# Kernel tuning notes

Hardware: AMD Instinct MI355X
Metric: run time of the kernel (lower is better)

Reference implementation:

```python
import jax, jax.numpy as jnp
import numpy as np

LOG2 = float(np.log(2.0))
N_NODES = 100000

def ssp(x):
    return jax.nn.softplus(x) - LOG2

def _xavier(key, out_dim, in_dim):
    bound = float(np.sqrt(6.0 / (in_dim + out_dim)))
    return jax.random.uniform(key, (out_dim, in_dim), jnp.float32, -bound, bound)

def setup_inputs() -> dict:
    key = jax.random.key(0)
    ks = jax.random.split(key, 10)
    H, F = 128, 128  # hidden_channels, num_filters
    C2 = int(2 * H * 0.5)          # lin2 out = 128
    C2h = int(2 * H) - C2          # lin2_hull out = 128
    E, Eh = 1600000, 400000
    v = jax.random.normal(ks[0], (N_NODES, H), jnp.float32)
    e = jax.random.normal(ks[1], (E, F), jnp.float32)
    edge_index = jax.random.randint(ks[2], (2, E), 0, N_NODES, jnp.int64)
    e_hull = jax.random.normal(ks[3], (Eh, F), jnp.float32)
    edge_index_hull = jax.random.randint(ks[4], (2, Eh), 0, N_NODES, jnp.int64)
    return {
        "v": v, "e": e, "edge_index": edge_index,
        "e_hull": e_hull, "edge_index_hull": edge_index_hull,
        "W1": _xavier(ks[5], H, F), "b1": jnp.zeros((H,), jnp.float32),
        "W2": _xavier(ks[6], C2, H), "b2": jnp.zeros((C2,), jnp.float32),
        "W1h": _xavier(ks[7], H, F), "b1h": jnp.zeros((H,), jnp.float32),
        "W2h": _xavier(ks[8], C2h, H), "b2h": jnp.zeros((C2h,), jnp.float32),
        "Wc": _xavier(ks[9], H, C2 + C2h), "bc": jnp.zeros((H,), jnp.float32),
    }

def reference(v, e, edge_index, e_hull, edge_index_hull,
              W1, b1, W2, b2, W1h, b1h, W2h, b2h, Wc, bc):
    n = v.shape[0]
    i = edge_index[1]
    out = jax.ops.segment_sum(e, i, num_segments=n)          # [N, F] scatter-sum
    out = ssp(out @ W1.T + b1) @ W2.T + b2                   # [N, C2]
    i_ = edge_index_hull[1]
    out_hull = jax.ops.segment_sum(e_hull, i_, num_segments=n)
    out_hull = ssp(out_hull @ W1h.T + b1h) @ W2h.T + b2h     # [N, C2h]
    cat = jnp.concatenate([out, out_hull], axis=1)           # [N, C2+C2h]
    return v + ssp(cat @ Wc.T + bc)
```

## Files before the change

### kernel.cpp

```cpp
#include <hip/hip_runtime.h>
#include <math.h>

typedef __attribute__((ext_vector_type(8))) short short8;
typedef __attribute__((ext_vector_type(4))) float f32x4;
typedef unsigned short u16;
typedef unsigned int u32;

__device__ __forceinline__ float ssp(float x) {
    const float LOG2E = 1.44269504088896340736f;
    const float LN2   = 0.69314718055994530942f;
    float t = __builtin_amdgcn_exp2f(-fabsf(x) * LOG2E);
    return fmaxf(x, 0.0f) + LN2 * __builtin_amdgcn_logf(1.0f + t) - LN2;
}

__device__ __forceinline__ u16 f2bf(float x) {
    u32 u = __float_as_uint(x);
    u32 r = (u + 0x7FFFu + ((u >> 16) & 1u)) >> 16;
    return (u16)r;
}

__global__ __launch_bounds__(256) void hist2_kernel(
    const int* __restrict__ tgt_m, int E,
    const int* __restrict__ tgt_h, int Eh,
    int* __restrict__ counts, int N)
{
    int i = blockIdx.x * 256 + threadIdx.x;
    if (i < E) atomicAdd(&counts[tgt_m[i]], 1);
    else if (i < E + Eh) atomicAdd(&counts[N + tgt_h[i - E]], 1);
}

__global__ __launch_bounds__(1024) void scan1_kernel(
    const int* __restrict__ counts, int* __restrict__ offsets,
    int* __restrict__ bsums, int n)
{
    __shared__ int buf[2][1024];
    const int tid = threadIdx.x;
    const int idx = blockIdx.x * 1024 + tid;
    int val = (idx < n) ? counts[idx] : 0;
    int cur = 0;
    buf[0][tid] = val;
    __syncthreads();
    for (int off = 1; off < 1024; off <<= 1) {
        int x = buf[cur][tid];
        if (tid >= off) x += buf[cur][tid - off];
        buf[cur ^ 1][tid] = x;
        cur ^= 1;
        __syncthreads();
    }
    if (idx < n) offsets[idx] = buf[cur][tid] - val;
    if (tid == 1023) bsums[blockIdx.x] = buf[cur][tid];
}

__global__ __launch_bounds__(256) void scan2_kernel(
    int* __restrict__ bsums, int nb, int* __restrict__ offsets, int n)
{
    __shared__ int b[2][256];
    const int tid = threadIdx.x;
    int val = (tid < nb) ? bsums[tid] : 0;
    int cur = 0;
    b[0][tid] = val;
    __syncthreads();
    for (int off = 1; off < 256; off <<= 1) {
        int x = b[cur][tid];
        if (tid >= off) x += b[cur][tid - off];
        b[cur ^ 1][tid] = x;
        cur ^= 1;
        __syncthreads();
    }
    if (tid < nb) bsums[tid] = b[cur][tid] - val;
    if (tid == 255) offsets[n] = b[cur][255];
}

__global__ __launch_bounds__(256) void scan3_kernel(
    int* __restrict__ offsets, const int* __restrict__ bsums, int n)
{
    int idx = blockIdx.x * 256 + threadIdx.x;
    if (idx < n) offsets[idx] += bsums[idx >> 10];
}

__global__ __launch_bounds__(256) void place2_kernel(
    const int* __restrict__ tgt_m, int E,
    const int* __restrict__ tgt_h, int Eh,
    const int* __restrict__ offsets, int* __restrict__ cursors,
    int* __restrict__ perm, int N)
{
    int i = blockIdx.x * 256 + threadIdx.x;
    if (i < E) {
        int slot = tgt_m[i];
        int pos = offsets[slot] + atomicAdd(&cursors[slot], 1);
        perm[pos] = i;
    } else if (i < E + Eh) {
        int slot = N + tgt_h[i - E];
        int pos = offsets[slot] + atomicAdd(&cursors[slot], 1);
        perm[pos] = i - E;
    }
}

__global__ __launch_bounds__(256) void wconvert_kernel(
    const float* __restrict__ W1, const float* __restrict__ W1h,
    const float* __restrict__ W2, const float* __restrict__ W2h,
    const float* __restrict__ Wc, u16* __restrict__ dst)
{
    int i = blockIdx.x * 256 + threadIdx.x;
    if (i >= 98304) return;
    const float* src; int off;
    if      (i < 16384) { src = W1;  off = i; }
    else if (i < 32768) { src = W1h; off = i - 16384; }
    else if (i < 49152) { src = W2;  off = i - 32768; }
    else if (i < 65536) { src = W2h; off = i - 49152; }
    else                { src = Wc;  off = i - 65536; }
    dst[i] = f2bf(src[off]);
}

#define MT 64

#define CHUNK_IDX(row, ch) (((row) * 16 + ((ch) ^ ((row) & 7))))
#define AFRAG(ls, row, ch) (*(const short8*)&(ls)[CHUNK_IDX(row, ch) * 8])

__device__ __forceinline__ f32x4 gather_rows(
    const f32x4* __restrict__ src, const int* __restrict__ perm,
    int k, int kend, int c4)
{
    f32x4 s = {0.f, 0.f, 0.f, 0.f};
    for (; k + 4 <= kend; k += 4) {
        int p0 = perm[k], p1 = perm[k + 1], p2 = perm[k + 2], p3 = perm[k + 3];
        f32x4 a = __builtin_nontemporal_load(&src[(size_t)p0 * 32 + c4]);
        f32x4 b = __builtin_nontemporal_load(&src[(size_t)p1 * 32 + c4]);
        f32x4 c = __builtin_nontemporal_load(&src[(size_t)p2 * 32 + c4]);
        f32x4 d = __builtin_nontemporal_load(&src[(size_t)p3 * 32 + c4]);
        s += (a + b) + (c + d);
    }
    for (; k + 2 <= kend; k += 2) {
        int p0 = perm[k], p1 = perm[k + 1];
        s += __builtin_nontemporal_load(&src[(size_t)p0 * 32 + c4])
           + __builtin_nontemporal_load(&src[(size_t)p1 * 32 + c4]);
    }
    if (k < kend)
        s += __builtin_nontemporal_load(&src[(size_t)perm[k] * 32 + c4]);
    return s;
}

__device__ __forceinline__ void layer128(
    u16* __restrict__ ls, const u16* __restrict__ W,
    const float* __restrict__ bias,
    int rw, int lr, int kc, bool act)
{
    const int arow = rw + lr;
    short8 af[4];
    #pragma unroll
    for (int s = 0; s < 4; s++) af[s] = AFRAG(ls, arow, s * 4 + kc);
    #pragma unroll
    for (int nt = 0; nt < 8; nt++) {
        const int bcol = nt * 16 + lr;
        const short8* wr = (const short8*)(W + bcol * 128);
        f32x4 acc = {0.f, 0.f, 0.f, 0.f};
        #pragma unroll
        for (int s = 0; s < 4; s++)
            acc = __builtin_amdgcn_mfma_f32_16x16x32_bf16(af[s], wr[s * 4 + kc], acc, 0, 0, 0);
        const float bn = bias[bcol];
        #pragma unroll
        for (int r = 0; r < 4; r++) {
            const int drow = rw + kc * 4 + r;
            float val = acc[r] + bn;
            if (act) val = ssp(val);
            ls[CHUNK_IDX(drow, bcol >> 3) * 8 + (bcol & 7)] = f2bf(val);
        }
    }
}

__global__ __launch_bounds__(256) void fused_mlp_kernel(
    const float* __restrict__ e, const float* __restrict__ eh,
    const int* __restrict__ perm, const int* __restrict__ offsets,
    const u16* __restrict__ Wbf,
    const float* __restrict__ b1, const float* __restrict__ b1h,
    const float* __restrict__ b2, const float* __restrict__ b2h,
    const float* __restrict__ bc,
    const float* __restrict__ v, float* __restrict__ out, int n)
{
    __shared__ __align__(16) u16 X0[MT * 128];
    __shared__ __align__(16) u16 X1[MT * 128];

    const int tid = threadIdx.x;
    const int l   = tid & 63;
    const int w   = tid >> 6;
    const int rw  = w * 16;
    const int lr  = l & 15;
    const int kc  = l >> 4;
    const int node0 = blockIdx.x * MT;

    const u16* W1  = Wbf;
    const u16* W1h = Wbf + 16384;
    const u16* W2  = Wbf + 32768;
    const u16* W2h = Wbf + 49152;
    const u16* Wc  = Wbf + 65536;

    const int hw = l >> 5;
    const int c4 = l & 31;
    const int ch = c4 >> 1;
    const int hf = (c4 & 1) * 4;
    for (int j = hw; j < 16; j += 2) {
        const int row  = rw + j;
        const int node = node0 + row;
        f32x4 sm = {0.f, 0.f, 0.f, 0.f};
        f32x4 sh = {0.f, 0.f, 0.f, 0.f};
        if (node < n) {
            sm = gather_rows((const f32x4*)e,  perm, offsets[node],     offsets[node + 1],     c4);
            sh = gather_rows((const f32x4*)eh, perm, offsets[n + node], offsets[n + node + 1], c4);
        }
        ushort4 om, oh;
        om.x = f2bf(sm.x); om.y = f2bf(sm.y); om.z = f2bf(sm.z); om.w = f2bf(sm.w);
        oh.x = f2bf(sh.x); oh.y = f2bf(sh.y); oh.z = f2bf(sh.z); oh.w = f2bf(sh.w);
        *(ushort4*)&X0[CHUNK_IDX(row, ch) * 8 + hf] = om;
        *(ushort4*)&X1[CHUNK_IDX(row, ch) * 8 + hf] = oh;
    }

    layer128(X0, W1,  b1,  rw, lr, kc, true);
    layer128(X1, W1h, b1h, rw, lr, kc, true);
    layer128(X0, W2,  b2,  rw, lr, kc, false);
    layer128(X1, W2h, b2h, rw, lr, kc, false);

    {
        const int arow = rw + lr;
        short8 af[8];
        #pragma unroll
        for (int s = 0; s < 4; s++) af[s]     = AFRAG(X0, arow, s * 4 + kc);
        #pragma unroll
        for (int s = 0; s < 4; s++) af[s + 4] = AFRAG(X1, arow, s * 4 + kc);
        #pragma unroll
        for (int nt = 0; nt < 8; nt++) {
            const int bcol = nt * 16 + lr;
            const short8* wr = (const short8*)(Wc + bcol * 256);
            f32x4 acc = {0.f, 0.f, 0.f, 0.f};
            #pragma unroll
            for (int s = 0; s < 8; s++)
                acc = __builtin_amdgcn_mfma_f32_16x16x32_bf16(af[s], wr[s * 4 + kc], acc, 0, 0, 0);
            const float bn = bc[bcol];
            #pragma unroll
            for (int r = 0; r < 4; r++) {
                const int drow = rw + kc * 4 + r;
                const int node = node0 + drow;
                if (node < n) {
                    size_t off = (size_t)node * 128 + bcol;
                    out[off] = v[off] + ssp(acc[r] + bn);
                }
            }
        }
    }
}

extern "C" void kernel_launch(void* const* d_in, const int* in_sizes, int n_in,
                              void* d_out, int out_size, void* d_ws, size_t ws_size,
                              hipStream_t stream)
{
    const float* v    = (const float*)d_in[0];
    const float* e    = (const float*)d_in[1];
    const int*   ei   = (const int*)  d_in[2];
    const float* eh   = (const float*)d_in[3];
    const int*   eih  = (const int*)  d_in[4];
    const float* W1   = (const float*)d_in[5];
    const float* b1   = (const float*)d_in[6];
    const float* W2   = (const float*)d_in[7];
    const float* b2   = (const float*)d_in[8];
    const float* W1h  = (const float*)d_in[9];
    const float* b1h  = (const float*)d_in[10];
    const float* W2h  = (const float*)d_in[11];
    const float* b2h  = (const float*)d_in[12];
    const float* Wc   = (const float*)d_in[13];
    const float* bc   = (const float*)d_in[14];
    float* out = (float*)d_out;

    const int N  = in_sizes[0] / 128;
    const int E  = (int)(in_sizes[1] / 128);
    const int Eh = (int)(in_sizes[3] / 128);
    const int n2 = 2 * N;

    u16* Wbf     = (u16*)d_ws;
    int* counts  = (int*)(Wbf + 98304);
    int* cursors = counts + n2;
    int* offsets = cursors + n2;
    int* bsums   = offsets + (n2 + 1);
    int* perm    = bsums + 256;

    const int* tgt_m = ei  + E;
    const int* tgt_h = eih + Eh;

    const int NB = (n2 + 1023) / 1024;
    const int ET = E + Eh;

    wconvert_kernel<<<(98304 + 255) / 256, 256, 0, stream>>>(W1, W1h, W2, W2h, Wc, Wbf);

    (void)hipMemsetAsync(counts, 0, (size_t)2 * n2 * 4, stream);
    hist2_kernel <<<(ET + 255) / 256, 256, 0, stream>>>(tgt_m, E, tgt_h, Eh, counts, N);
    scan1_kernel <<<NB, 1024, 0, stream>>>(counts, offsets, bsums, n2);
    scan2_kernel <<<1, 256, 0, stream>>>(bsums, NB, offsets, n2);
    scan3_kernel <<<(n2 + 255) / 256, 256, 0, stream>>>(offsets, bsums, n2);
    place2_kernel<<<(ET + 255) / 256, 256, 0, stream>>>(tgt_m, E, tgt_h, Eh, offsets, cursors, perm, N);

    fused_mlp_kernel<<<(N + MT - 1) / MT, 256, 0, stream>>>(
        e, eh, perm, offsets, Wbf, b1, b1h, b2, b2h, bc, v, out, N);
}
```

Before: 607.6 us.

## Fuse all stages into one cooperative persistent kernel with grid syncs

Replaces the weight-convert, memset, histogram, three scan, placement and fused MLP launches with a single cooperative kernel that separates phases with grid.sync. The grid is sized from the occupancy query and each phase uses grid-stride or persistent tile loops, so the per-launch gaps and the separate memset go away. The scan is reorganised to 512 elements per block with 256 threads. The edge gather loop is also unrolled from 4 to 8 loads to keep more memory requests in flight. In exchange it pays for several grid-wide barriers, ties the tile count to resident blocks, and may use more registers, which can lower occupancy in the gather-heavy MLP phase.

```diff
diff --git a/kernel.cpp b/kernel.cpp
--- a/kernel.cpp
+++ b/kernel.cpp
@@ -1,5 +1,8 @@
 #include <hip/hip_runtime.h>
+#include <hip/hip_cooperative_groups.h>
 #include <math.h>
+
+namespace cg = cooperative_groups;
 
 typedef __attribute__((ext_vector_type(8))) short short8;
 typedef __attribute__((ext_vector_type(4))) float f32x4;
@@ -19,116 +22,32 @@
     return (u16)r;
 }
 
-__global__ __launch_bounds__(256) void hist2_kernel(
-    const int* __restrict__ tgt_m, int E,
-    const int* __restrict__ tgt_h, int Eh,
-    int* __restrict__ counts, int N)
-{
-    int i = blockIdx.x * 256 + threadIdx.x;
-    if (i < E) atomicAdd(&counts[tgt_m[i]], 1);
-    else if (i < E + Eh) atomicAdd(&counts[N + tgt_h[i - E]], 1);
-}
-
-__global__ __launch_bounds__(1024) void scan1_kernel(
-    const int* __restrict__ counts, int* __restrict__ offsets,
-    int* __restrict__ bsums, int n)
-{
-    __shared__ int buf[2][1024];
-    const int tid = threadIdx.x;
-    const int idx = blockIdx.x * 1024 + tid;
-    int val = (idx < n) ? counts[idx] : 0;
-    int cur = 0;
-    buf[0][tid] = val;
-    __syncthreads();
-    for (int off = 1; off < 1024; off <<= 1) {
-        int x = buf[cur][tid];
-        if (tid >= off) x += buf[cur][tid - off];
-        buf[cur ^ 1][tid] = x;
-        cur ^= 1;
-        __syncthreads();
-    }
-    if (idx < n) offsets[idx] = buf[cur][tid] - val;
-    if (tid == 1023) bsums[blockIdx.x] = buf[cur][tid];
-}
-
-__global__ __launch_bounds__(256) void scan2_kernel(
-    int* __restrict__ bsums, int nb, int* __restrict__ offsets, int n)
-{
-    __shared__ int b[2][256];
-    const int tid = threadIdx.x;
-    int val = (tid < nb) ? bsums[tid] : 0;
-    int cur = 0;
-    b[0][tid] = val;
-    __syncthreads();
-    for (int off = 1; off < 256; off <<= 1) {
-        int x = b[cur][tid];
-        if (tid >= off) x += b[cur][tid - off];
-        b[cur ^ 1][tid] = x;
-        cur ^= 1;
-        __syncthreads();
-    }
-    if (tid < nb) bsums[tid] = b[cur][tid] - val;
-    if (tid == 255) offsets[n] = b[cur][255];
-}
-
-__global__ __launch_bounds__(256) void scan3_kernel(
-    int* __restrict__ offsets, const int* __restrict__ bsums, int n)
-{
-    int idx = blockIdx.x * 256 + threadIdx.x;
-    if (idx < n) offsets[idx] += bsums[idx >> 10];
-}
-
-__global__ __launch_bounds__(256) void place2_kernel(
-    const int* __restrict__ tgt_m, int E,
-    const int* __restrict__ tgt_h, int Eh,
-    const int* __restrict__ offsets, int* __restrict__ cursors,
-    int* __restrict__ perm, int N)
-{
-    int i = blockIdx.x * 256 + threadIdx.x;
-    if (i < E) {
-        int slot = tgt_m[i];
-        int pos = offsets[slot] + atomicAdd(&cursors[slot], 1);
-        perm[pos] = i;
-    } else if (i < E + Eh) {
-        int slot = N + tgt_h[i - E];
-        int pos = offsets[slot] + atomicAdd(&cursors[slot], 1);
-        perm[pos] = i - E;
-    }
-}
-
-__global__ __launch_bounds__(256) void wconvert_kernel(
-    const float* __restrict__ W1, const float* __restrict__ W1h,
-    const float* __restrict__ W2, const float* __restrict__ W2h,
-    const float* __restrict__ Wc, u16* __restrict__ dst)
-{
-    int i = blockIdx.x * 256 + threadIdx.x;
-    if (i >= 98304) return;
-    const float* src; int off;
-    if      (i < 16384) { src = W1;  off = i; }
-    else if (i < 32768) { src = W1h; off = i - 16384; }
-    else if (i < 49152) { src = W2;  off = i - 32768; }
-    else if (i < 65536) { src = W2h; off = i - 49152; }
-    else                { src = Wc;  off = i - 65536; }
-    dst[i] = f2bf(src[off]);
-}
-
-#define MT 64
-
-#define CHUNK_IDX(row, ch) (((row) * 16 + ((ch) ^ ((row) & 7))))
-#define AFRAG(ls, row, ch) (*(const short8*)&(ls)[CHUNK_IDX(row, ch) * 8])
+struct MegaArgs {
+    const float *v, *e;
+    const int   *ei;
+    const float *eh;
+    const int   *eih;
+    const float *W1, *b1, *W2, *b2, *W1h, *b1h, *W2h, *b2h, *Wc, *bc;
+    float* out;
+    u16* Wbf;
+    int *counts, *cursors, *offsets, *bsums, *perm;
+    int N, E, Eh;
+};
 
 __device__ __forceinline__ f32x4 gather_rows(
     const f32x4* __restrict__ src, const int* __restrict__ perm,
     int k, int kend, int c4)
 {
     f32x4 s = {0.f, 0.f, 0.f, 0.f};
-    for (; k + 4 <= kend; k += 4) {
-        int p0 = perm[k], p1 = perm[k + 1], p2 = perm[k + 2], p3 = perm[k + 3];
-        f32x4 a = __builtin_nontemporal_load(&src[(size_t)p0 * 32 + c4]);
-        f32x4 b = __builtin_nontemporal_load(&src[(size_t)p1 * 32 + c4]);
-        f32x4 c = __builtin_nontemporal_load(&src[(size_t)p2 * 32 + c4]);
-        f32x4 d = __builtin_nontemporal_load(&src[(size_t)p3 * 32 + c4]);
-        s += (a + b) + (c + d);
+    for (; k + 8 <= kend; k += 8) {
+        int p[8];
+        #pragma unroll
+        for (int q = 0; q < 8; q++) p[q] = perm[k + q];
+        f32x4 r[8];
+        #pragma unroll
+        for (int q = 0; q < 8; q++)
+            r[q] = __builtin_nontemporal_load(&src[(size_t)p[q] * 32 + c4]);
+        s += ((r[0] + r[1]) + (r[2] + r[3])) + ((r[4] + r[5]) + (r[6] + r[7]));
     }
     for (; k + 2 <= kend; k += 2) {
         int p0 = perm[k], p1 = perm[k + 1];
@@ -139,6 +58,9 @@
         s += __builtin_nontemporal_load(&src[(size_t)perm[k] * 32 + c4]);
     return s;
 }
+
+#define CHUNK_IDX(row, ch) (((row) * 16 + ((ch) ^ ((row) & 7))))
+#define AFRAG(ls, row, ch) (*(const short8*)&(ls)[CHUNK_IDX(row, ch) * 8])
 
 __device__ __forceinline__ void layer128(
     u16* __restrict__ ls, const u16* __restrict__ W,
@@ -168,80 +90,172 @@
     }
 }
 
-__global__ __launch_bounds__(256) void fused_mlp_kernel(
-    const float* __restrict__ e, const float* __restrict__ eh,
-    const int* __restrict__ perm, const int* __restrict__ offsets,
-    const u16* __restrict__ Wbf,
-    const float* __restrict__ b1, const float* __restrict__ b1h,
-    const float* __restrict__ b2, const float* __restrict__ b2h,
-    const float* __restrict__ bc,
-    const float* __restrict__ v, float* __restrict__ out, int n)
-{
-    __shared__ __align__(16) u16 X0[MT * 128];
-    __shared__ __align__(16) u16 X1[MT * 128];
-
+__device__ __forceinline__ int block_incl_scan(int val, int tid, int* sb)
+{
+    int cur = 0;
+    sb[tid] = val;
+    __syncthreads();
+    #pragma unroll
+    for (int off = 1; off < 256; off <<= 1) {
+        int x = sb[cur * 256 + tid];
+        if (tid >= off) x += sb[cur * 256 + tid - off];
+        sb[(cur ^ 1) * 256 + tid] = x;
+        cur ^= 1;
+        __syncthreads();
+    }
+    return sb[cur * 256 + tid];
+}
+
+__global__ __launch_bounds__(256) void mega_kernel(MegaArgs a)
+{
+    __shared__ __align__(16) u16 X0[64 * 128];
+    __shared__ __align__(16) u16 X1[64 * 128];
+
+    cg::grid_group grid = cg::this_grid();
     const int tid = threadIdx.x;
-    const int l   = tid & 63;
-    const int w   = tid >> 6;
-    const int rw  = w * 16;
-    const int lr  = l & 15;
-    const int kc  = l >> 4;
-    const int node0 = blockIdx.x * MT;
-
-    const u16* W1  = Wbf;
-    const u16* W1h = Wbf + 16384;
-    const u16* W2  = Wbf + 32768;
-    const u16* W2h = Wbf + 49152;
-    const u16* Wc  = Wbf + 65536;
-
+    const int bid = blockIdx.x;
+    const int G   = gridDim.x;
+    const int gsz = G * 256;
+    const int gtid = bid * 256 + tid;
+    const int N = a.N, E = a.E, Eh = a.Eh;
+    const int n2 = 2 * N;
+    const int* tgt_m = a.ei  + E;
+    const int* tgt_h = a.eih + Eh;
+
+    for (int i = gtid; i < 98304; i += gsz) {
+        const float* src; int off;
+        if      (i < 16384) { src = a.W1;  off = i; }
+        else if (i < 32768) { src = a.W1h; off = i - 16384; }
+        else if (i < 49152) { src = a.W2;  off = i - 32768; }
+        else if (i < 65536) { src = a.W2h; off = i - 49152; }
+        else                { src = a.Wc;  off = i - 65536; }
+        a.Wbf[i] = f2bf(src[off]);
+    }
+    for (int i = gtid; i < 2 * n2; i += gsz) a.counts[i] = 0;
+    grid.sync();
+
+    for (int i = gtid; i < E + Eh; i += gsz) {
+        if (i < E) atomicAdd(&a.counts[tgt_m[i]], 1);
+        else       atomicAdd(&a.counts[N + tgt_h[i - E]], 1);
+    }
+    grid.sync();
+
+    int* sbuf = (int*)X0;
+    const int NBC = (n2 + 511) / 512;
+    for (int c = bid; c < NBC; c += G) {
+        const int base = c * 512;
+        const int i0 = base + 2 * tid, i1 = i0 + 1;
+        int v0 = (i0 < n2) ? a.counts[i0] : 0;
+        int v1 = (i1 < n2) ? a.counts[i1] : 0;
+        int incl = block_incl_scan(v0 + v1, tid, sbuf);
+        int excl = incl - (v0 + v1);
+        if (i0 < n2) a.offsets[i0] = excl;
+        if (i1 < n2) a.offsets[i1] = excl + v0;
+        if (tid == 255) a.bsums[c] = incl;
+        __syncthreads();
+    }
+    grid.sync();
+
+    if (bid == 0) {
+        const int i0 = 2 * tid, i1 = i0 + 1;
+        int v0 = (i0 < NBC) ? a.bsums[i0] : 0;
+        int v1 = (i1 < NBC) ? a.bsums[i1] : 0;
+        int incl = block_incl_scan(v0 + v1, tid, sbuf);
+        int excl = incl - (v0 + v1);
+        if (i0 < NBC) a.bsums[i0] = excl;
+        if (i1 < NBC) a.bsums[i1] = excl + v0;
+        if (tid == 255) a.offsets[n2] = incl;
+    }
+    grid.sync();
+
+    for (int c = bid; c < NBC; c += G) {
+        const int add = a.bsums[c];
+        const int base = c * 512;
+        const int lim = (base + 512 < n2) ? base + 512 : n2;
+        for (int i = base + tid; i < lim; i += 256) a.offsets[i] += add;
+    }
+    grid.sync();
+
+    for (int i = gtid; i < E + Eh; i += gsz) {
+        if (i < E) {
+            int slot = tgt_m[i];
+            int pos = a.offsets[slot] + atomicAdd(&a.cursors[slot], 1);
+            a.perm[pos] = i;
+        } else {
+            int slot = N + tgt_h[i - E];
+            int pos = a.offsets[slot] + atomicAdd(&a.cursors[slot], 1);
+            a.perm[pos] = i - E;
+        }
+    }
+    grid.sync();
+
+    const u16* W1  = a.Wbf;
+    const u16* W1h = a.Wbf + 16384;
+    const u16* W2  = a.Wbf + 32768;
+    const u16* W2h = a.Wbf + 49152;
+    const u16* Wc  = a.Wbf + 65536;
+
+    const int l  = tid & 63;
+    const int w  = tid >> 6;
+    const int rw = w * 16;
+    const int lr = l & 15;
+    const int kc = l >> 4;
     const int hw = l >> 5;
     const int c4 = l & 31;
     const int ch = c4 >> 1;
     const int hf = (c4 & 1) * 4;
-    for (int j = hw; j < 16; j += 2) {
-        const int row  = rw + j;
-        const int node = node0 + row;
-        f32x4 sm = {0.f, 0.f, 0.f, 0.f};
-        f32x4 sh = {0.f, 0.f, 0.f, 0.f};
-        if (node < n) {
-            sm = gather_rows((const f32x4*)e,  perm, offsets[node],     offsets[node + 1],     c4);
-            sh = gather_rows((const f32x4*)eh, perm, offsets[n + node], offsets[n + node + 1], c4);
+    const int NT = (N + 63) / 64;
+
+    for (int t = bid; t < NT; t += G) {
+        const int node0 = t * 64;
+
+        for (int j = hw; j < 16; j += 2) {
+            const int row  = rw + j;
+            const int node = node0 + row;
+            f32x4 sm = {0.f, 0.f, 0.f, 0.f};
+            f32x4 sh = {0.f, 0.f, 0.f, 0.f};
+            if (node < N) {
+                int s0m = a.offsets[node],     s1m = a.offsets[node + 1];
+                int s0h = a.offsets[N + node], s1h = a.offsets[N + node + 1];
+                sm = gather_rows((const f32x4*)a.e,  a.perm, s0m, s1m, c4);
+                sh = gather_rows((const f32x4*)a.eh, a.perm, s0h, s1h, c4);
+            }
+            ushort4 om, oh;
+            om.x = f2bf(sm.x); om.y = f2bf(sm.y); om.z = f2bf(sm.z); om.w = f2bf(sm.w);
+            oh.x = f2bf(sh.x); oh.y = f2bf(sh.y); oh.z = f2bf(sh.z); oh.w = f2bf(sh.w);
+            *(ushort4*)&X0[CHUNK_IDX(row, ch) * 8 + hf] = om;
+            *(ushort4*)&X1[CHUNK_IDX(row, ch) * 8 + hf] = oh;
         }
-        ushort4 om, oh;
-        om.x = f2bf(sm.x); om.y = f2bf(sm.y); om.z = f2bf(sm.z); om.w = f2bf(sm.w);
-        oh.x = f2bf(sh.x); oh.y = f2bf(sh.y); oh.z = f2bf(sh.z); oh.w = f2bf(sh.w);
-        *(ushort4*)&X0[CHUNK_IDX(row, ch) * 8 + hf] = om;
-        *(ushort4*)&X1[CHUNK_IDX(row, ch) * 8 + hf] = oh;
-    }
-
-    layer128(X0, W1,  b1,  rw, lr, kc, true);
-    layer128(X1, W1h, b1h, rw, lr, kc, true);
-    layer128(X0, W2,  b2,  rw, lr, kc, false);
-    layer128(X1, W2h, b2h, rw, lr, kc, false);
-
-    {
-        const int arow = rw + lr;
-        short8 af[8];
-        #pragma unroll
-        for (int s = 0; s < 4; s++) af[s]     = AFRAG(X0, arow, s * 4 + kc);
-        #pragma unroll
-        for (int s = 0; s < 4; s++) af[s + 4] = AFRAG(X1, arow, s * 4 + kc);
-        #pragma unroll
-        for (int nt = 0; nt < 8; nt++) {
-            const int bcol = nt * 16 + lr;
-            const short8* wr = (const short8*)(Wc + bcol * 256);
-            f32x4 acc = {0.f, 0.f, 0.f, 0.f};
+
+        layer128(X0, W1,  a.b1,  rw, lr, kc, true);
+        layer128(X1, W1h, a.b1h, rw, lr, kc, true);
+        layer128(X0, W2,  a.b2,  rw, lr, kc, false);
+        layer128(X1, W2h, a.b2h, rw, lr, kc, false);
+
+        {
+            const int arow = rw + lr;
+            short8 af[8];
             #pragma unroll
-            for (int s = 0; s < 8; s++)
-                acc = __builtin_amdgcn_mfma_f32_16x16x32_bf16(af[s], wr[s * 4 + kc], acc, 0, 0, 0);
-            const float bn = bc[bcol];
+            for (int s = 0; s < 4; s++) af[s]     = AFRAG(X0, arow, s * 4 + kc);
             #pragma unroll
-            for (int r = 0; r < 4; r++) {
-                const int drow = rw + kc * 4 + r;
-                const int node = node0 + drow;
-                if (node < n) {
-                    size_t off = (size_t)node * 128 + bcol;
-                    out[off] = v[off] + ssp(acc[r] + bn);
+            for (int s = 0; s < 4; s++) af[s + 4] = AFRAG(X1, arow, s * 4 + kc);
+            #pragma unroll
+            for (int nt = 0; nt < 8; nt++) {
+                const int bcol = nt * 16 + lr;
+                const short8* wr = (const short8*)(Wc + bcol * 256);
+                f32x4 acc = {0.f, 0.f, 0.f, 0.f};
+                #pragma unroll
+                for (int s = 0; s < 8; s++)
+                    acc = __builtin_amdgcn_mfma_f32_16x16x32_bf16(af[s], wr[s * 4 + kc], acc, 0, 0, 0);
+                const float bn = a.bc[bcol];
+                #pragma unroll
+                for (int r = 0; r < 4; r++) {
+                    const int drow = rw + kc * 4 + r;
+                    const int node = node0 + drow;
+                    if (node < N) {
+                        size_t off = (size_t)node * 128 + bcol;
+                        a.out[off] = a.v[off] + ssp(acc[r] + bn);
+                    }
                 }
             }
         }
@@ -252,50 +266,42 @@
                               void* d_out, int out_size, void* d_ws, size_t ws_size,
                               hipStream_t stream)
 {
-    const float* v    = (const float*)d_in[0];
-    const float* e    = (const float*)d_in[1];
-    const int*   ei   = (const int*)  d_in[2];
-    const float* eh   = (const float*)d_in[3];
-    const int*   eih  = (const int*)  d_in[4];
-    const float* W1   = (const float*)d_in[5];
-    const float* b1   = (const float*)d_in[6];
-    const float* W2   = (const float*)d_in[7];
-    const float* b2   = (const float*)d_in[8];
-    const float* W1h  = (const float*)d_in[9];
-    const float* b1h  = (const float*)d_in[10];
-    const float* W2h  = (const float*)d_in[11];
-    const float* b2h  = (const float*)d_in[12];
-    const float* Wc   = (const float*)d_in[13];
-    const float* bc   = (const float*)d_in[14];
-    float* out = (float*)d_out;
-
-    const int N  = in_sizes[0] / 128;
-    const int E  = (int)(in_sizes[1] / 128);
-    const int Eh = (int)(in_sizes[3] / 128);
-    const int n2 = 2 * N;
-
-    u16* Wbf     = (u16*)d_ws;
-    int* counts  = (int*)(Wbf + 98304);
-    int* cursors = counts + n2;
-    int* offsets = cursors + n2;
-    int* bsums   = offsets + (n2 + 1);
-    int* perm    = bsums + 256;
-
-    const int* tgt_m = ei  + E;
-    const int* tgt_h = eih + Eh;
-
-    const int NB = (n2 + 1023) / 1024;
-    const int ET = E + Eh;
-
-    wconvert_kernel<<<(98304 + 255) / 256, 256, 0, stream>>>(W1, W1h, W2, W2h, Wc, Wbf);
-
-    (void)hipMemsetAsync(counts, 0, (size_t)2 * n2 * 4, stream);
-    hist2_kernel <<<(ET + 255) / 256, 256, 0, stream>>>(tgt_m, E, tgt_h, Eh, counts, N);
-    scan1_kernel <<<NB, 1024, 0, stream>>>(counts, offsets, bsums, n2);
-    scan2_kernel <<<1, 256, 0, stream>>>(bsums, NB, offsets, n2);
-    scan3_kernel <<<(n2 + 255) / 256, 256, 0, stream>>>(offsets, bsums, n2);
-    place2_kernel<<<(ET + 255) / 256, 256, 0, stream>>>(tgt_m, E, tgt_h, Eh, offsets, cursors, perm, N);
-
-    fused_mlp_kernel<<<(N + MT - 1) / MT, 256, 0, stream>>>(
-        e, eh, perm, offsets, Wbf, b1, b1h, b2, b2h, bc, v, out, N);
-}
+    MegaArgs a;
+    a.v    = (const float*)d_in[0];
+    a.e    = (const float*)d_in[1];
+    a.ei   = (const int*)  d_in[2];
+    a.eh   = (const float*)d_in[3];
+    a.eih  = (const int*)  d_in[4];
+    a.W1   = (const float*)d_in[5];
+    a.b1   = (const float*)d_in[6];
+    a.W2   = (const float*)d_in[7];
+    a.b2   = (const float*)d_in[8];
+    a.W1h  = (const float*)d_in[9];
+    a.b1h  = (const float*)d_in[10];
+    a.W2h  = (const float*)d_in[11];
+    a.b2h  = (const float*)d_in[12];
+    a.Wc   = (const float*)d_in[13];
+    a.bc   = (const float*)d_in[14];
+    a.out  = (float*)d_out;
+
+    a.N  = in_sizes[0] / 128;
+    a.E  = (int)(in_sizes[1] / 128);
+    a.Eh = (int)(in_sizes[3] / 128);
+    const int n2 = 2 * a.N;
+
+    a.Wbf     = (u16*)d_ws;
+    a.counts  = (int*)(a.Wbf + 98304);
+    a.cursors = a.counts + n2;
+    a.offsets = a.cursors + n2;
+    a.bsums   = a.offsets + (n2 + 1);
+    a.perm    = a.bsums + 512;
+
+    int bpc = 0;
+    (void)hipOccupancyMaxActiveBlocksPerMultiprocessor(&bpc, mega_kernel, 256, 0);
+    if (bpc < 1) bpc = 1;
+    int G = bpc * 256;
+    if (G > 4096) G = 4096;
+
+    void* ka[] = { (void*)&a };
+    (void)hipLaunchCooperativeKernel((void*)mega_kernel, dim3(G), dim3(256), ka, 0, stream);
+}
```

Measured after the change: 1.054 ms. +73.5%, slower.
